# Performance work log

Measured on AMD Instinct MI355X. Metric: run time of the kernel, lower is better.

The kernel has to match this reference:

```python
import jax, jax.numpy as jnp
import numpy as np


def setup_inputs() -> dict:
    key = jax.random.key(0)
    k1, k2, k3, k4, k5 = jax.random.split(key, 5)
    B, S, D, F, E = 4, 4096, 1024, 2048, 8
    top_k = 2
    num_tokens = B * S
    capacity = max(int(num_tokens / E * 1.25), 4)  # 2560
    scale = 0.02
    return {
        "x": jax.random.normal(k1, (B, S, D), dtype=jnp.float32),
        "gate_w": jax.random.normal(k2, (D, E), dtype=jnp.float32) * scale,
        "w_gate": jax.random.normal(k3, (E, D, F), dtype=jnp.float32) * scale,
        "w_up": jax.random.normal(k4, (E, D, F), dtype=jnp.float32) * scale,
        "w_down": jax.random.normal(k5, (E, F, D), dtype=jnp.float32) * scale,
        "num_experts": E,
        "top_k": top_k,
        "capacity": capacity,
    }


AUX_LOSS_WEIGHT = 0.01


def reference(x, gate_w, w_gate, w_up, w_down, num_experts, top_k, capacity):
    B, S, D = x.shape
    N = B * S
    x_flat = x.reshape(N, D)

    # ---- Router ----
    logits = x_flat @ gate_w                      # [N, E]
    probs = jax.nn.softmax(logits, axis=-1)
    weights, indices = jax.lax.top_k(probs, top_k)  # [N, K]
    weights = weights / jnp.sum(weights, axis=-1, keepdims=True)

    # ---- Capacity-based dispatch ----
    indices_flat = indices.reshape(-1)            # [N*K]
    x_rep = jnp.repeat(x_flat, top_k, axis=0)     # [N*K, D]
    expert_mask = jax.nn.one_hot(indices_flat, num_experts, dtype=jnp.int32)  # [N*K, E]
    token_priority = jnp.cumsum(expert_mask, axis=0) * expert_mask
    token_rank = jnp.sum(token_priority, axis=1)  # [N*K], 1-based rank within expert
    valid = (token_rank > 0) & (token_rank <= capacity)
    gather_idx = indices_flat * capacity + (token_rank - 1)  # [N*K]

    total_slots = num_experts * capacity
    # drop-mode scatter: invalid rows are sent out-of-bounds and dropped
    safe_idx = jnp.where(valid, gather_idx, total_slots)
    dispatched = jnp.zeros((total_slots, D), dtype=x.dtype)
    dispatched = dispatched.at[safe_idx].set(x_rep, mode="drop")
    dispatched = dispatched.reshape(num_experts, capacity, D)  # [E, C, D]

    # ---- Fused experts (grouped BMM, SwiGLU) ----
    gate = jnp.einsum("ecd,edf->ecf", dispatched, w_gate)
    up = jnp.einsum("ecd,edf->ecf", dispatched, w_up)
    hidden = jax.nn.silu(gate) * up
    expert_out = jnp.einsum("ecf,efd->ecd", hidden, w_down)
    expert_out_flat = expert_out.reshape(total_slots, D)

    # ---- Combine (row-aligned gather; dropped tokens contribute zero) ----
    gathered = expert_out_flat[jnp.clip(gather_idx, 0, total_slots - 1)]
    combined = jnp.where(valid[:, None], gathered, jnp.zeros((), dtype=x.dtype))
    combined = combined.reshape(N, top_k, D)
    output = jnp.sum(combined * weights[:, :, None], axis=1)  # [N, D]

    # ---- Aux load-balance loss ----
    mask = jax.nn.one_hot(indices, num_experts, dtype=jnp.float32).sum(axis=1)  # [N, E]
    f = mask.sum(axis=0) / (N * top_k + 1e-9)
    P = probs.mean(axis=0)
    aux_loss = num_experts * jnp.sum(f * P) * AUX_LOSS_WEIGHT

    return output.reshape(B, S, D), aux_loss
```

## Files before the change

kernel.cpp:

```cpp
#include <hip/hip_runtime.h>
#include <stdint.h>

#define N_TOK 16384
#define DIM   1024
#define NEXP  8
#define FF    2048
#define CAP   2560
#define NSLOT (NEXP*CAP)

using f32x4  = __attribute__((ext_vector_type(4))) float;
using bf16x8 = __attribute__((ext_vector_type(8))) short;

__device__ __forceinline__ unsigned short f2bf(float f){
  union { float f; unsigned u; } c; c.f = f;
  unsigned u = c.u + 0x7FFFu + ((c.u >> 16) & 1u);
  return (unsigned short)(u >> 16);
}
__device__ __forceinline__ float bf2f(unsigned short h){
  union { unsigned u; float f; } c; c.u = ((unsigned)h) << 16; return c.f;
}

__device__ __forceinline__ void gld16(const unsigned short* g, unsigned short* l){
  __builtin_amdgcn_global_load_lds((__attribute__((address_space(1))) void*)(void*)g,
                                   (__attribute__((address_space(3))) void*)l,
                                   16, 0, 0);
}

#define SBAR __builtin_amdgcn_sched_barrier(0)
#define HBAR __builtin_amdgcn_s_barrier()
#define LG0  asm volatile("s_waitcnt lgkmcnt(0)" ::: "memory")

__global__ __launch_bounds__(256) void k_router(
    const float* __restrict__ x, const float* __restrict__ gate_w,
    float* __restrict__ probs, int* __restrict__ topidx, float* __restrict__ topw)
{
  __shared__ float gwT[NEXP][DIM];
  int tid = threadIdx.x;
  for (int i = tid; i < DIM*NEXP; i += 256) gwT[i & 7][i >> 3] = gate_w[i];
  __syncthreads();
  int wave = tid >> 6, lane = tid & 63;
  int t = blockIdx.x * 4 + wave;
  const float* xr = x + (size_t)t * DIM;
  double acc[NEXP];
  #pragma unroll
  for (int e = 0; e < NEXP; e++) acc[e] = 0.0;
  for (int j = 0; j < DIM/64; j++){
    double xv = (double)xr[lane + 64*j];
    #pragma unroll
    for (int e = 0; e < NEXP; e++) acc[e] += xv * (double)gwT[e][lane + 64*j];
  }
  #pragma unroll
  for (int off = 32; off >= 1; off >>= 1){
    #pragma unroll
    for (int e = 0; e < NEXP; e++) acc[e] += __shfl_xor(acc[e], off, 64);
  }
  if (lane == 0){
    double m = acc[0];
    #pragma unroll
    for (int e = 1; e < NEXP; e++) m = fmax(m, acc[e]);
    double p[NEXP], Z = 0.0;
    #pragma unroll
    for (int e = 0; e < NEXP; e++){ p[e] = exp(acc[e] - m); Z += p[e]; }
    double invZ = 1.0 / Z;
    #pragma unroll
    for (int e = 0; e < NEXP; e++){ p[e] *= invZ; probs[t*NEXP + e] = (float)p[e]; }
    int i0 = 0; double p0 = p[0];
    #pragma unroll
    for (int e = 1; e < NEXP; e++) if (p[e] > p0){ p0 = p[e]; i0 = e; }
    int i1 = (i0 == 0) ? 1 : 0; double p1 = p[i1];
    #pragma unroll
    for (int e = 0; e < NEXP; e++) if (e != i0 && p[e] > p1){ p1 = p[e]; i1 = e; }
    double s = p0 + p1;
    topidx[t*2+0] = i0; topidx[t*2+1] = i1;
    topw [t*2+0] = (float)(p0/s); topw[t*2+1] = (float)(p1/s);
  }
}

__global__ __launch_bounds__(1024) void k_scan(
    const int* __restrict__ topidx,
    int* __restrict__ slot_token, int* __restrict__ tok_slots,
    int* __restrict__ counts_total)
{
  __shared__ int sc[1024][NEXP];
  const int t = threadIdx.x;
  const int base_i = t * 32;
  int ids[32];
  #pragma unroll
  for (int j = 0; j < 32; j++) ids[j] = topidx[base_i + j];
  int b[NEXP];
  #pragma unroll
  for (int e = 0; e < NEXP; e++) b[e] = 0;
  #pragma unroll
  for (int j = 0; j < 32; j++){
    #pragma unroll
    for (int e = 0; e < NEXP; e++) if (ids[j] == e) b[e]++;
  }
  #pragma unroll
  for (int e = 0; e < NEXP; e++) sc[t][e] = b[e];
  __syncthreads();
  for (int off = 1; off < 1024; off <<= 1){
    int tmp[NEXP];
    #pragma unroll
    for (int e = 0; e < NEXP; e++) tmp[e] = (t >= off) ? sc[t-off][e] : 0;
    __syncthreads();
    #pragma unroll
    for (int e = 0; e < NEXP; e++) sc[t][e] += tmp[e];
    __syncthreads();
  }
  int myb[NEXP];
  #pragma unroll
  for (int e = 0; e < NEXP; e++) myb[e] = sc[t][e] - b[e];
  if (t == 1023){
    #pragma unroll
    for (int e = 0; e < NEXP; e++) counts_total[e] = sc[1023][e];
  }
  #pragma unroll
  for (int j = 0; j < 32; j++){
    int slot = -1;
    #pragma unroll
    for (int e = 0; e < NEXP; e++){
      if (ids[j] == e){
        int r = myb[e]; myb[e] = r + 1;
        if (r < CAP){
          slot = e*CAP + r;
          slot_token[slot] = (base_i + j) >> 1;
        }
      }
    }
    tok_slots[base_i + j] = slot;
  }
}

template<int MODE>
__global__ __launch_bounds__(256) void k_tc(
    const float* __restrict__ in, unsigned short* __restrict__ out,
    int R, int C, size_t estride)
{
  __shared__ float tile[64][65];
  const int e  = blockIdx.z;
  const float* ine = in + (size_t)e * R * C;
  unsigned short* oute = out + (size_t)e * estride;
  const int c0 = blockIdx.x * 64, r0 = blockIdx.y * 64;
  const int tx = threadIdx.x & 63, ty = threadIdx.x >> 6;
  #pragma unroll
  for (int i = 0; i < 16; i++){
    int r = ty*16 + i;
    tile[r][tx] = ine[(size_t)(r0 + r) * C + c0 + tx];
  }
  __syncthreads();
  #pragma unroll
  for (int i = 0; i < 16; i++){
    int c = c0 + ty*16 + i;
    int orow = (MODE == 0) ? ((c>>4)*32 + (c&15))
             : (MODE == 1) ? ((c>>4)*32 + 16 + (c&15))
             : c;
    oute[(size_t)orow * R + r0 + tx] = f2bf(tile[tx][ty*16 + i]);
  }
}

__global__ __launch_bounds__(256) void k_gather(
    const float* __restrict__ x, const int* __restrict__ slot_token,
    unsigned short* __restrict__ disp)
{
  const int s = blockIdx.x;
  const int t = slot_token[s];
  const int tid = threadIdx.x;
  unsigned long long pk = 0ull;
  if (t >= 0){
    float4 v = *(const float4*)(x + (size_t)t*DIM + tid*4);
    pk =  (unsigned long long)f2bf(v.x)
       | ((unsigned long long)f2bf(v.y) << 16)
       | ((unsigned long long)f2bf(v.z) << 32)
       | ((unsigned long long)f2bf(v.w) << 48);
  }
  *(unsigned long long*)(disp + (size_t)s*DIM + tid*4) = pk;
}

__device__ __forceinline__ void stg(const unsigned short* gsrc, int ldg,
                                    unsigned short* Lh, int wave, int lane){
  const int sl = (lane & 3) ^ ((lane >> 3) & 3);
  #pragma unroll
  for (int j = 0; j < 2; j++){
    int bi = wave*2 + j;
    gld16(gsrc + (size_t)(bi*16 + (lane >> 2))*ldg + sl*8, Lh + bi*512);
  }
}
__device__ __forceinline__ bf16x8 frd(const unsigned short* Lh, int r, int g){
  return *(const bf16x8*)(Lh + r*32 + (((g ^ ((r >> 1) & 3))) << 3));
}
template<int MG>
__device__ __forceinline__ void mm16(f32x4 (&acc)[8][4], const bf16x8 (&a)[4], const bf16x8 (&b)[4]){
  #pragma unroll
  for (int i = 0; i < 4; i++)
    #pragma unroll
    for (int n = 0; n < 4; n++)
      acc[MG*4+i][n] = __builtin_amdgcn_mfma_f32_16x16x32_bf16(a[i], b[n], acc[MG*4+i][n], 0, 0, 0);
}

#define HALF_STEP(RS, DOSTG, VMW, ASRC, BSRC)                                   \
  {                                                                             \
    unsigned short* LA = lds + (RS)*16384;                                      \
    unsigned short* LB = LA + 8192;                                             \
    unsigned short* NS = lds + (((RS)+3)&3)*16384;                              \
    bf16x8 a[4], b[4];                                                          \
    _Pragma("unroll")                                                           \
    for (int i = 0; i < 4; i++) a[i] = frd(LA, wr*128 + i*16 + l15, g);         \
    _Pragma("unroll")                                                           \
    for (int n = 0; n < 4; n++) b[n] = frd(LB, wc*64 + n*16 + l15, g);          \
    if (DOSTG) stg(ASRC, KDIM, NS, wave, lane);                                 \
    SBAR; HBAR; LG0; SBAR;                                                      \
    __builtin_amdgcn_s_setprio(1);  mm16<0>(acc, a, b);                         \
    __builtin_amdgcn_s_setprio(0);                                              \
    SBAR; HBAR; SBAR;                                                           \
    _Pragma("unroll")                                                           \
    for (int i = 0; i < 4; i++) a[i] = frd(LA, wr*128 + (4+i)*16 + l15, g);     \
    if (DOSTG) stg(BSRC, KDIM, NS + 8192, wave, lane);                          \
    SBAR; HBAR; LG0; SBAR;                                                      \
    __builtin_amdgcn_s_setprio(1);  mm16<1>(acc, a, b);                         \
    __builtin_amdgcn_s_setprio(0);                                              \
    if ((VMW) == 8) { asm volatile("s_waitcnt vmcnt(8)" ::: "memory"); }        \
    else if ((VMW) == 4) { asm volatile("s_waitcnt vmcnt(4)" ::: "memory"); }   \
    else if ((VMW) == 0) { asm volatile("s_waitcnt vmcnt(0)" ::: "memory"); }   \
    SBAR; HBAR; SBAR;                                                           \
  }

template<int KDIM, int EPI>
__global__ __launch_bounds__(512, 2) void k_gemm8(
    const unsigned short* __restrict__ A,
    const unsigned short* __restrict__ B,
    unsigned short* __restrict__ Out)
{
  constexpr int NH    = KDIM / 32;
  constexpr int BROWS = (EPI == 1) ? 2*FF : DIM;
  constexpr int LDO   = (EPI == 1) ? FF : DIM;
  __shared__ unsigned short lds[65536];
  const int id = blockIdx.x;
  const int e  = id & 7;
  const int t  = id >> 3;
  const int mt = t % 10, nt = t / 10;
  const int m0 = mt*256, n0 = nt*256;
  const unsigned short* Ab = A + ((size_t)e*CAP   + m0) * KDIM;
  const unsigned short* Bb = B + ((size_t)e*BROWS + n0) * KDIM;
  const int tid = threadIdx.x, wave = tid >> 6, lane = tid & 63;
  const int wr = wave >> 2, wc = wave & 3;
  const int g = lane >> 4, l15 = lane & 15;

  f32x4 acc[8][4];
  const f32x4 z4 = {0.f,0.f,0.f,0.f};
  #pragma unroll
  for (int i = 0; i < 8; i++)
    #pragma unroll
    for (int n = 0; n < 4; n++) acc[i][n] = z4;

  stg(Ab,      KDIM, lds + 0*16384,        wave, lane);
  stg(Bb,      KDIM, lds + 0*16384 + 8192, wave, lane);
  stg(Ab + 32, KDIM, lds + 1*16384,        wave, lane);
  stg(Bb + 32, KDIM, lds + 1*16384 + 8192, wave, lane);
  stg(Ab + 64, KDIM, lds + 2*16384,        wave, lane);
  stg(Bb + 64, KDIM, lds + 2*16384 + 8192, wave, lane);
  asm volatile("s_waitcnt vmcnt(8)" ::: "memory");
  SBAR; HBAR; SBAR;

  for (int h = 0; h + 8 <= NH; h += 4){
    HALF_STEP(0, true, 8, Ab + (size_t)(h+3)*32, Bb + (size_t)(h+3)*32);
    HALF_STEP(1, true, 8, Ab + (size_t)(h+4)*32, Bb + (size_t)(h+4)*32);
    HALF_STEP(2, true, 8, Ab + (size_t)(h+5)*32, Bb + (size_t)(h+5)*32);
    HALF_STEP(3, true, 8, Ab + (size_t)(h+6)*32, Bb + (size_t)(h+6)*32);
  }
  HALF_STEP(0, true,  8, Ab + (size_t)(NH-1)*32, Bb + (size_t)(NH-1)*32);
  HALF_STEP(1, false, 4, Ab, Bb);
  HALF_STEP(2, false, 0, Ab, Bb);
  HALF_STEP(3, false, -1, Ab, Bb);

  if (EPI == 1){
    unsigned short* H = Out + ((size_t)e*CAP + m0 + wr*128) * (size_t)LDO;
    const int hc0 = (n0 + wc*64) >> 1;
    #pragma unroll
    for (int mf = 0; mf < 8; mf++)
      #pragma unroll
      for (int q = 0; q < 4; q++){
        int r = mf*16 + g*4 + q;
        #pragma unroll
        for (int p = 0; p < 2; p++){
          float gg = acc[mf][2*p][q], uu = acc[mf][2*p+1][q];
          float h = gg / (1.f + __expf(-gg)) * uu;
          H[(size_t)r*LDO + hc0 + p*16 + l15] = f2bf(h);
        }
      }
  } else {
    unsigned short* O = Out + ((size_t)e*CAP + m0 + wr*128) * (size_t)LDO + n0 + wc*64;
    #pragma unroll
    for (int mf = 0; mf < 8; mf++)
      #pragma unroll
      for (int q = 0; q < 4; q++){
        int r = mf*16 + g*4 + q;
        #pragma unroll
        for (int n = 0; n < 4; n++)
          O[(size_t)r*LDO + n*16 + l15] = f2bf(acc[mf][n][q]);
      }
  }
}

__global__ __launch_bounds__(128) void k_combine(
    const unsigned short* __restrict__ slot_out, const int* __restrict__ tok_slots,
    const float* __restrict__ topw, float* __restrict__ out)
{
  const int t = blockIdx.x, tid = threadIdx.x;
  const int s0 = tok_slots[t*2+0], s1 = tok_slots[t*2+1];
  const float w0 = topw[t*2+0], w1 = topw[t*2+1];
  float r[8];
  #pragma unroll
  for (int j = 0; j < 8; j++) r[j] = 0.f;
  if (s0 >= 0){
    bf16x8 v = *(const bf16x8*)(slot_out + (size_t)s0*DIM + tid*8);
    #pragma unroll
    for (int j = 0; j < 8; j++) r[j] += w0 * bf2f((unsigned short)v[j]);
  }
  if (s1 >= 0){
    bf16x8 v = *(const bf16x8*)(slot_out + (size_t)s1*DIM + tid*8);
    #pragma unroll
    for (int j = 0; j < 8; j++) r[j] += w1 * bf2f((unsigned short)v[j]);
  }
  float4* o = (float4*)(out + (size_t)t*DIM + tid*8);
  o[0] = make_float4(r[0], r[1], r[2], r[3]);
  o[1] = make_float4(r[4], r[5], r[6], r[7]);
}

__global__ __launch_bounds__(256) void k_aux(
    const float* __restrict__ probs, const int* __restrict__ counts_total,
    float* __restrict__ aux_out)
{
  const int tid = threadIdx.x;
  float pe[NEXP];
  #pragma unroll
  for (int e = 0; e < NEXP; e++) pe[e] = 0.f;
  for (int i = tid; i < N_TOK; i += 256){
    #pragma unroll
    for (int e = 0; e < NEXP; e++) pe[e] += probs[i*NEXP + e];
  }
  #pragma unroll
  for (int off = 32; off >= 1; off >>= 1){
    #pragma unroll
    for (int e = 0; e < NEXP; e++) pe[e] += __shfl_xor(pe[e], off, 64);
  }
  __shared__ float part[4][NEXP];
  const int wave = tid >> 6, lane = tid & 63;
  if (lane == 0){
    #pragma unroll
    for (int e = 0; e < NEXP; e++) part[wave][e] = pe[e];
  }
  __syncthreads();
  if (tid == 0){
    float aux = 0.f;
    for (int e = 0; e < NEXP; e++){
      float P = (part[0][e] + part[1][e] + part[2][e] + part[3][e]) / (float)N_TOK;
      float f = (float)counts_total[e] / ((float)(N_TOK*2) + 1e-9f);
      aux += f * P;
    }
    aux_out[0] = (float)NEXP * aux * 0.01f;
  }
}

extern "C" void kernel_launch(void* const* d_in, const int* in_sizes, int n_in,
                              void* d_out, int out_size, void* d_ws, size_t ws_size,
                              hipStream_t stream)
{
  const float* x      = (const float*)d_in[0];
  const float* gate_w = (const float*)d_in[1];
  const float* w_gate = (const float*)d_in[2];
  const float* w_up   = (const float*)d_in[3];
  const float* w_down = (const float*)d_in[4];
  float* out = (float*)d_out;

  uint8_t* ws = (uint8_t*)d_ws;
  float* probs        = (float*)ws;             ws += (size_t)N_TOK*NEXP*4;
  int*   topidx       = (int*)ws;               ws += (size_t)N_TOK*2*4;
  float* topw         = (float*)ws;             ws += (size_t)N_TOK*2*4;
  int*   slot_token   = (int*)ws;               ws += (size_t)NSLOT*4;
  int*   tok_slots    = (int*)ws;               ws += (size_t)N_TOK*2*4;
  int*   counts_total = (int*)ws;               ws += 256;
  unsigned short* disp   = (unsigned short*)ws; ws += (size_t)NSLOT*DIM*2;
  unsigned short* hidden = (unsigned short*)ws; ws += (size_t)NSLOT*FF*2;
  unsigned short* B1     = (unsigned short*)ws; ws += (size_t)NEXP*2*FF*DIM*2;
  unsigned short* wdT    = (unsigned short*)ws; ws += (size_t)NEXP*DIM*FF*2;
  size_t need = (size_t)(ws - (uint8_t*)d_ws);
  if (ws_size < need) return;
  unsigned short* slot_out = disp;

  hipMemsetAsync(slot_token, 0xFF, (size_t)NSLOT * sizeof(int), stream);

  k_router<<<N_TOK/4, 256, 0, stream>>>(x, gate_w, probs, topidx, topw);
  k_scan<<<1, 1024, 0, stream>>>(topidx, slot_token, tok_slots, counts_total);
  k_tc<0><<<dim3(FF/64, DIM/64, NEXP), 256, 0, stream>>>(w_gate, B1, DIM, FF, (size_t)2*FF*DIM);
  k_tc<1><<<dim3(FF/64, DIM/64, NEXP), 256, 0, stream>>>(w_up,   B1, DIM, FF, (size_t)2*FF*DIM);
  k_tc<2><<<dim3(DIM/64, FF/64, NEXP), 256, 0, stream>>>(w_down, wdT, FF, DIM, (size_t)DIM*FF);
  k_gather<<<NSLOT, 256, 0, stream>>>(x, slot_token, disp);
  k_gemm8<DIM, 1><<<1280, 512, 0, stream>>>(disp, B1, hidden);
  k_gemm8<FF, 2><<<320, 512, 0, stream>>>(hidden, wdT, slot_out);
  k_combine<<<N_TOK, 128, 0, stream>>>(slot_out, tok_slots, topw, out);
  k_aux<<<1, 256, 0, stream>>>(probs, counts_total, out + (size_t)N_TOK*DIM);
}
```

Baseline: 506.5 us.

## Vectorize weight transpose, retune GEMM waits, drop sched barriers, widen combine blocks

The weight transpose kernel now loads float4 and writes packed 8-byte bf16 stores to cut memory transaction count. The GEMM pipeline drops the scheduling barriers and changes the vmcnt waits to fire every other half-step with a tighter count, which changes how much load latency overlaps with MFMA. The combine kernel processes two tokens per 256-thread block. Removing the sched barriers lets the compiler reorder LDS reads and MFMAs, but the sparser waits could let a stage be read before its load lands if the counts are off.

```diff
diff --git a/kernel.cpp b/kernel.cpp
--- a/kernel.cpp
+++ b/kernel.cpp
@@ -26,7 +26,6 @@
                                    16, 0, 0);
 }
 
-#define SBAR __builtin_amdgcn_sched_barrier(0)
 #define HBAR __builtin_amdgcn_s_barrier()
 #define LG0  asm volatile("s_waitcnt lgkmcnt(0)" ::: "memory")
 
@@ -132,29 +131,40 @@
 }
 
 template<int MODE>
-__global__ __launch_bounds__(256) void k_tc(
+__global__ __launch_bounds__(256) void k_tcv(
     const float* __restrict__ in, unsigned short* __restrict__ out,
     int R, int C, size_t estride)
 {
-  __shared__ float tile[64][65];
+  __shared__ float tt[64][65];
   const int e  = blockIdx.z;
   const float* ine = in + (size_t)e * R * C;
   unsigned short* oute = out + (size_t)e * estride;
   const int c0 = blockIdx.x * 64, r0 = blockIdx.y * 64;
-  const int tx = threadIdx.x & 63, ty = threadIdx.x >> 6;
-  #pragma unroll
-  for (int i = 0; i < 16; i++){
-    int r = ty*16 + i;
-    tile[r][tx] = ine[(size_t)(r0 + r) * C + c0 + tx];
+  const int tid = threadIdx.x;
+  #pragma unroll
+  for (int i = 0; i < 4; i++){
+    int idx = i*256 + tid;
+    int row = idx >> 4, c4 = idx & 15;
+    float4 v = *(const float4*)(ine + (size_t)(r0 + row)*C + c0 + c4*4);
+    tt[c4*4+0][row] = v.x; tt[c4*4+1][row] = v.y;
+    tt[c4*4+2][row] = v.z; tt[c4*4+3][row] = v.w;
   }
   __syncthreads();
   #pragma unroll
-  for (int i = 0; i < 16; i++){
-    int c = c0 + ty*16 + i;
+  for (int i = 0; i < 2; i++){
+    int cl = i*32 + (tid >> 3);
+    int rs = (tid & 7) * 8;
+    int c  = c0 + cl;
     int orow = (MODE == 0) ? ((c>>4)*32 + (c&15))
              : (MODE == 1) ? ((c>>4)*32 + 16 + (c&15))
              : c;
-    oute[(size_t)orow * R + r0 + tx] = f2bf(tile[tx][ty*16 + i]);
+    unsigned long long pk0 = 0, pk1 = 0;
+    #pragma unroll
+    for (int j = 0; j < 4; j++) pk0 |= (unsigned long long)f2bf(tt[cl][rs+j]) << (16*j);
+    #pragma unroll
+    for (int j = 0; j < 4; j++) pk1 |= (unsigned long long)f2bf(tt[cl][rs+4+j]) << (16*j);
+    unsigned long long* dst = (unsigned long long*)(oute + (size_t)orow*R + r0 + rs);
+    dst[0] = pk0; dst[1] = pk1;
   }
 }
 
@@ -208,20 +218,19 @@
     _Pragma("unroll")                                                           \
     for (int n = 0; n < 4; n++) b[n] = frd(LB, wc*64 + n*16 + l15, g);          \
     if (DOSTG) stg(ASRC, KDIM, NS, wave, lane);                                 \
-    SBAR; HBAR; LG0; SBAR;                                                      \
+    HBAR; LG0;                                                                  \
     __builtin_amdgcn_s_setprio(1);  mm16<0>(acc, a, b);                         \
     __builtin_amdgcn_s_setprio(0);                                              \
-    SBAR; HBAR; SBAR;                                                           \
+    HBAR;                                                                       \
     _Pragma("unroll")                                                           \
     for (int i = 0; i < 4; i++) a[i] = frd(LA, wr*128 + (4+i)*16 + l15, g);     \
     if (DOSTG) stg(BSRC, KDIM, NS + 8192, wave, lane);                          \
-    SBAR; HBAR; LG0; SBAR;                                                      \
+    HBAR; LG0;                                                                  \
     __builtin_amdgcn_s_setprio(1);  mm16<1>(acc, a, b);                         \
     __builtin_amdgcn_s_setprio(0);                                              \
-    if ((VMW) == 8) { asm volatile("s_waitcnt vmcnt(8)" ::: "memory"); }        \
-    else if ((VMW) == 4) { asm volatile("s_waitcnt vmcnt(4)" ::: "memory"); }   \
+    if ((VMW) == 4) { asm volatile("s_waitcnt vmcnt(4)" ::: "memory"); }        \
     else if ((VMW) == 0) { asm volatile("s_waitcnt vmcnt(0)" ::: "memory"); }   \
-    SBAR; HBAR; SBAR;                                                           \
+    HBAR;                                                                       \
   }
 
 template<int KDIM, int EPI>
@@ -258,18 +267,18 @@
   stg(Bb + 32, KDIM, lds + 1*16384 + 8192, wave, lane);
   stg(Ab + 64, KDIM, lds + 2*16384,        wave, lane);
   stg(Bb + 64, KDIM, lds + 2*16384 + 8192, wave, lane);
-  asm volatile("s_waitcnt vmcnt(8)" ::: "memory");
-  SBAR; HBAR; SBAR;
+  asm volatile("s_waitcnt vmcnt(4)" ::: "memory");
+  HBAR;
 
   for (int h = 0; h + 8 <= NH; h += 4){
-    HALF_STEP(0, true, 8, Ab + (size_t)(h+3)*32, Bb + (size_t)(h+3)*32);
-    HALF_STEP(1, true, 8, Ab + (size_t)(h+4)*32, Bb + (size_t)(h+4)*32);
-    HALF_STEP(2, true, 8, Ab + (size_t)(h+5)*32, Bb + (size_t)(h+5)*32);
-    HALF_STEP(3, true, 8, Ab + (size_t)(h+6)*32, Bb + (size_t)(h+6)*32);
-  }
-  HALF_STEP(0, true,  8, Ab + (size_t)(NH-1)*32, Bb + (size_t)(NH-1)*32);
-  HALF_STEP(1, false, 4, Ab, Bb);
-  HALF_STEP(2, false, 0, Ab, Bb);
+    HALF_STEP(0, true, -1, Ab + (size_t)(h+3)*32, Bb + (size_t)(h+3)*32);
+    HALF_STEP(1, true,  4, Ab + (size_t)(h+4)*32, Bb + (size_t)(h+4)*32);
+    HALF_STEP(2, true, -1, Ab + (size_t)(h+5)*32, Bb + (size_t)(h+5)*32);
+    HALF_STEP(3, true,  4, Ab + (size_t)(h+6)*32, Bb + (size_t)(h+6)*32);
+  }
+  HALF_STEP(0, true, -1, Ab + (size_t)(NH-1)*32, Bb + (size_t)(NH-1)*32);
+  HALF_STEP(1, false, 0, Ab, Bb);
+  HALF_STEP(2, false, -1, Ab, Bb);
   HALF_STEP(3, false, -1, Ab, Bb);
 
   if (EPI == 1){
@@ -301,11 +310,12 @@
   }
 }
 
-__global__ __launch_bounds__(128) void k_combine(
+__global__ __launch_bounds__(256) void k_combine(
     const unsigned short* __restrict__ slot_out, const int* __restrict__ tok_slots,
     const float* __restrict__ topw, float* __restrict__ out)
 {
-  const int t = blockIdx.x, tid = threadIdx.x;
+  const int t = blockIdx.x*2 + (threadIdx.x >> 7);
+  const int tid = threadIdx.x & 127;
   const int s0 = tok_slots[t*2+0], s1 = tok_slots[t*2+1];
   const float w0 = topw[t*2+0], w1 = topw[t*2+1];
   float r[8];
@@ -391,12 +401,12 @@
 
   k_router<<<N_TOK/4, 256, 0, stream>>>(x, gate_w, probs, topidx, topw);
   k_scan<<<1, 1024, 0, stream>>>(topidx, slot_token, tok_slots, counts_total);
-  k_tc<0><<<dim3(FF/64, DIM/64, NEXP), 256, 0, stream>>>(w_gate, B1, DIM, FF, (size_t)2*FF*DIM);
-  k_tc<1><<<dim3(FF/64, DIM/64, NEXP), 256, 0, stream>>>(w_up,   B1, DIM, FF, (size_t)2*FF*DIM);
-  k_tc<2><<<dim3(DIM/64, FF/64, NEXP), 256, 0, stream>>>(w_down, wdT, FF, DIM, (size_t)DIM*FF);
+  k_tcv<0><<<dim3(FF/64, DIM/64, NEXP), 256, 0, stream>>>(w_gate, B1, DIM, FF, (size_t)2*FF*DIM);
+  k_tcv<1><<<dim3(FF/64, DIM/64, NEXP), 256, 0, stream>>>(w_up,   B1, DIM, FF, (size_t)2*FF*DIM);
+  k_tcv<2><<<dim3(DIM/64, FF/64, NEXP), 256, 0, stream>>>(w_down, wdT, FF, DIM, (size_t)DIM*FF);
   k_gather<<<NSLOT, 256, 0, stream>>>(x, slot_token, disp);
   k_gemm8<DIM, 1><<<1280, 512, 0, stream>>>(disp, B1, hidden);
   k_gemm8<FF, 2><<<320, 512, 0, stream>>>(hidden, wdT, slot_out);
-  k_combine<<<N_TOK, 128, 0, stream>>>(slot_out, tok_slots, topw, out);
+  k_combine<<<N_TOK/2, 256, 0, stream>>>(slot_out, tok_slots, topw, out);
   k_aux<<<1, 256, 0, stream>>>(probs, counts_total, out + (size_t)N_TOK*DIM);
 }
```

Result: no change. 508.8 us (+0.4%).
